# Optimization experiments

Measured on AMD Instinct MI355X. Metric: run time of the kernel, lower is better.

The kernel has to match this reference:

```python
import jax, jax.numpy as jnp
import numpy as np

B, D, T, V = 16, 128, 4096, 1024


def setup_inputs() -> dict:
    key = jax.random.key(0)
    k1, k2 = jax.random.split(key)
    latents = jax.random.normal(k1, (B, D, T), dtype=jnp.float32)
    codebook = jax.random.normal(k2, (V, D), dtype=jnp.float32)  # code_embed.weight
    return {"latents": latents, "codebook": codebook}


def reference(latents, codebook):
    # decode(): latents (B, D, T) -> (B, T, D); nearest code under L2 (torch.cdist + argmin)
    x = jnp.transpose(latents, (0, 2, 1))  # (B, T, D)
    x_sq = jnp.sum(x * x, axis=-1, keepdims=True)          # (B, T, 1)
    c_sq = jnp.sum(codebook * codebook, axis=-1)           # (V,)
    cross = jnp.einsum('btd,vd->btv', x, codebook)         # (B, T, V) -- the fusion target
    d2 = x_sq - 2.0 * cross + c_sq                         # (B, T, V)
    codes = jnp.argmin(d2, axis=-1)                        # (B, T) int
    # quantized latents: embed the chosen codes back to (B, D, T)
    quantized = jnp.transpose(codebook[codes], (0, 2, 1))  # (B, D, T)
    return codes.astype(jnp.int32), quantized
```

## Files before the change

kernel.cpp:

```cpp
#include <hip/hip_runtime.h>

#define B_ 16
#define D_ 128
#define T_ 4096
#define V_ 1024

typedef _Float16 half8 __attribute__((ext_vector_type(8)));
typedef float float4v __attribute__((ext_vector_type(4)));


__global__ __launch_bounds__(256) void split_csq_kernel(const float* __restrict__ cb,
                                                        _Float16* __restrict__ Bh,
                                                        _Float16* __restrict__ Bl,
                                                        float* __restrict__ chsq) {
    const int g = blockIdx.x * 256 + threadIdx.x;
    const int v = g >> 4;
    const int k0 = (g & 15) << 3;
    const float* src = cb + (size_t)v * D_ + k0;
    half8 h, l;
    float s = 0.f;
#pragma unroll
    for (int j = 0; j < 8; ++j) {
        float c = src[j];
        _Float16 ch = (_Float16)c;
        h[j] = ch;
        l[j] = (_Float16)((c - (float)ch) * 2048.0f);
        s = fmaf(c, c, s);
    }
    const int kt = k0 >> 5;
    const int kk = k0 & 31;
    const size_t off = ((size_t)(kt * V_ + v)) * 32 + kk;
    *(half8*)(Bh + off) = h;
    *(half8*)(Bl + off) = l;
#pragma unroll
    for (int o = 1; o < 16; o <<= 1) s += __shfl_xor(s, o, 64);
    if ((g & 15) == 0) chsq[v] = 0.5f * s;
}

__device__ __forceinline__ void dma16(const char* g, char* lds) {
    __builtin_amdgcn_global_load_lds(
        (const __attribute__((address_space(1))) unsigned int*)g,
        (__attribute__((address_space(3))) unsigned int*)lds, 16, 0, 0);
}

__device__ __forceinline__ void dma_chunk(char* ldsbuf, const char* BhB, const char* BlB,
                                          int c, int wv, int swoff) {
#pragma unroll
    for (int j = 0; j < 2; ++j) {
        const int seg = wv * 2 + j;
        const int hl = seg >> 3;
        const int kt = (seg >> 1) & 3;
        const char* src = (hl ? BlB : BhB) + kt * 65536 + c * 2048 + j * 1024 + swoff;
        dma16(src, ldsbuf + seg * 1024);
    }
}

__global__ __launch_bounds__(512, 4) void vq_mfma(const float* __restrict__ latents,
                                                  const float* __restrict__ codebook,
                                                  const float* __restrict__ chsq,
                                                  const _Float16* __restrict__ Bh,
                                                  const _Float16* __restrict__ Bl,
                                                  float* __restrict__ out_codes,
                                                  float* __restrict__ out_q) {
    __shared__ __align__(16) char smem[69632];
    __shared__ float sChsq[V_];
    __shared__ int scode[128];
    __shared__ float sBestF[2][128];
    __shared__ int sBestV[2][128];

    const int tid = threadIdx.x;
    const int tl = tid & 63;
    const int wv = tid >> 6;
    const int wt = wv & 3;
    const int wn = wv >> 2;
    const int ln = tid & 15;
    const int q = (tid >> 4) & 3;
    const int b = blockIdx.x >> 5;
    const int t00 = (blockIdx.x & 31) << 7;

    const int swoff = ((tl >> 2) << 6) + ((((tl & 3) ^ ((tl >> 3) & 3))) << 4);
    const int qs16 = ((q ^ ((ln >> 1) & 3)) << 4);

    _Float16* AhS = (_Float16*)smem;
    _Float16* AlS = AhS + 128 * 136;

#pragma unroll
    for (int i = 0; i < V_ / 512; ++i) sChsq[tid + i * 512] = chsq[tid + i * 512];

    {
        const int arow = tid & 127;
        const int adh = tid >> 7;
        const float* xp = latents + (size_t)b * D_ * T_ + t00 + arow;
#pragma unroll
        for (int i = 0; i < 4; ++i) {
            const int d0 = adh * 32 + i * 8;
            float x[8];
#pragma unroll
            for (int j = 0; j < 8; ++j) x[j] = xp[(size_t)(d0 + j) * T_];
            half8 h, l;
#pragma unroll
            for (int j = 0; j < 8; ++j) {
                _Float16 xh = (_Float16)x[j];
                h[j] = xh;
                l[j] = (_Float16)((x[j] - (float)xh) * 2048.0f);
            }
            *(half8*)(AhS + arow * 136 + d0) = h;
            *(half8*)(AlS + arow * 136 + d0) = l;
        }
    }
    __syncthreads();

    half8 ah[4][2], al[4][2];
#pragma unroll
    for (int kt = 0; kt < 4; ++kt)
#pragma unroll
        for (int mt = 0; mt < 2; ++mt) {
            const int row = wt * 32 + mt * 16 + ln;
            ah[kt][mt] = *(const half8*)(AhS + row * 136 + kt * 32 + q * 8);
            al[kt][mt] = *(const half8*)(AlS + row * 136 + kt * 32 + q * 8);
        }
    __syncthreads();

    char* Bb = smem;
    const char* BhB = (const char*)Bh;
    const char* BlB = (const char*)Bl;

    float bestF[2][4];
    int bestv[2][4];
#pragma unroll
    for (int mt = 0; mt < 2; ++mt)
#pragma unroll
        for (int r = 0; r < 4; ++r) {
            bestF[mt][r] = 3.0e38f;
            bestv[mt][r] = 0;
        }

    dma_chunk(Bb + 0 * 16384, BhB, BlB, 0, wv, swoff);
    dma_chunk(Bb + 1 * 16384, BhB, BlB, 1, wv, swoff);
    dma_chunk(Bb + 2 * 16384, BhB, BlB, 2, wv, swoff);

    for (int c = 0; c < 32; ++c) {
        asm volatile("s_waitcnt vmcnt(4)" ::: "memory");
        __builtin_amdgcn_s_barrier();
        asm volatile("" ::: "memory");

        dma_chunk(Bb + ((c + 3) & 3) * 16384, BhB, BlB, (c + 3) & 31, wv, swoff);

        const char* buf = Bb + (c & 3) * 16384;
        float4v acc1[2], acc2[2];
#pragma unroll
        for (int mt = 0; mt < 2; ++mt) {
            acc1[mt] = (float4v){0.f, 0.f, 0.f, 0.f};
            acc2[mt] = (float4v){0.f, 0.f, 0.f, 0.f};
        }
        __builtin_amdgcn_s_setprio(1);
#pragma unroll
        for (int kt = 0; kt < 4; ++kt) {
            const int o = kt * 2048 + (wn * 16 + ln) * 64 + qs16;
            const half8 bh = *(const half8*)(buf + o);
            const half8 bl = *(const half8*)(buf + 8192 + o);
#pragma unroll
            for (int mt = 0; mt < 2; ++mt) {
                acc1[mt] = __builtin_amdgcn_mfma_f32_16x16x32_f16(ah[kt][mt], bh,
                                                                  acc1[mt], 0, 0, 0);
                acc2[mt] = __builtin_amdgcn_mfma_f32_16x16x32_f16(ah[kt][mt], bl,
                                                                  acc2[mt], 0, 0, 0);
                acc2[mt] = __builtin_amdgcn_mfma_f32_16x16x32_f16(al[kt][mt], bh,
                                                                  acc2[mt], 0, 0, 0);
            }
        }
        __builtin_amdgcn_s_setprio(0);
        {
            const int n = c * 32 + wn * 16 + ln;
            const float csq = sChsq[n];
#pragma unroll
            for (int mt = 0; mt < 2; ++mt)
#pragma unroll
                for (int r = 0; r < 4; ++r) {
                    const float score =
                        csq - (acc1[mt][r] + acc2[mt][r] * (1.0f / 2048.0f));
                    if (score < bestF[mt][r]) {
                        bestF[mt][r] = score;
                        bestv[mt][r] = n;
                    }
                }
        }
    }

#pragma unroll
    for (int off = 1; off < 16; off <<= 1) {
#pragma unroll
        for (int mt = 0; mt < 2; ++mt)
#pragma unroll
            for (int r = 0; r < 4; ++r) {
                const float of = __shfl_xor(bestF[mt][r], off, 64);
                const int ov = __shfl_xor(bestv[mt][r], off, 64);
                if (of < bestF[mt][r] || (of == bestF[mt][r] && ov < bestv[mt][r])) {
                    bestF[mt][r] = of;
                    bestv[mt][r] = ov;
                }
            }
    }

    if (ln == 0) {
#pragma unroll
        for (int mt = 0; mt < 2; ++mt)
#pragma unroll
            for (int r = 0; r < 4; ++r) {
                const int m = wt * 32 + mt * 16 + q * 4 + r;
                sBestF[wn][m] = bestF[mt][r];
                sBestV[wn][m] = bestv[mt][r];
            }
    }
    __syncthreads();

    if (tid < 128) {
        const float f0 = sBestF[0][tid];
        const float f1 = sBestF[1][tid];
        const int v0 = sBestV[0][tid];
        const int v1 = sBestV[1][tid];
        const int vb = (f1 < f0 || (f1 == f0 && v1 < v0)) ? v1 : v0;
        scode[tid] = vb;
        out_codes[(size_t)b * T_ + t00 + tid] = (float)vb;
    }
    __syncthreads();

    {
        const int row = tid & 127;
        const int dq = tid >> 7;
        const int code = scode[row];
        const float* crow = codebook + (size_t)code * D_;
        float* qp = out_q + (size_t)b * D_ * T_ + t00 + row;
#pragma unroll
        for (int i = 0; i < 32; ++i) {
            const int d = dq * 32 + i;
            qp[(size_t)d * T_] = crow[d];
        }
    }
}

extern "C" void kernel_launch(void* const* d_in, const int* in_sizes, int n_in,
                              void* d_out, int out_size, void* d_ws, size_t ws_size,
                              hipStream_t stream) {
    const float* latents = (const float*)d_in[0];
    const float* codebook = (const float*)d_in[1];

    float* out_codes = (float*)d_out;
    float* out_q = (float*)d_out + B_ * T_;

    float* chsq = (float*)d_ws;
    _Float16* Bh = (_Float16*)((char*)d_ws + 4096);
    _Float16* Bl = (_Float16*)((char*)d_ws + 4096 + 262144);

    split_csq_kernel<<<(V_ * 16) / 256, 256, 0, stream>>>(codebook, Bh, Bl, chsq);
    vq_mfma<<<(B_ * T_) / 128, 512, 0, stream>>>(latents, codebook, chsq, Bh, Bl,
                                                 out_codes, out_q);
}
```

Measured before the change: 137.1 us.

## Process two codebook chunks per barrier and fold -|c|^2 into accumulator init

The main loop now handles two 32-code chunks per iteration. It waits on vmcnt(0) with one barrier per pair instead of one per chunk, and prefetch depth drops from three chunks to two. The -|c|^2 term now seeds the MFMA accumulator, so the argmin becomes an argmax over the accumulated value and a subtract per element goes away. The occupancy hint in launch_bounds is removed, which lets the compiler use more registers but may reduce waves per CU, and the full vmcnt wait can expose more load latency.

```diff
diff --git a/kernel.cpp b/kernel.cpp
--- a/kernel.cpp
+++ b/kernel.cpp
@@ -55,17 +55,17 @@
     }
 }
 
-__global__ __launch_bounds__(512, 4) void vq_mfma(const float* __restrict__ latents,
-                                                  const float* __restrict__ codebook,
-                                                  const float* __restrict__ chsq,
-                                                  const _Float16* __restrict__ Bh,
-                                                  const _Float16* __restrict__ Bl,
-                                                  float* __restrict__ out_codes,
-                                                  float* __restrict__ out_q) {
+__global__ __launch_bounds__(512) void vq_mfma(const float* __restrict__ latents,
+                                               const float* __restrict__ codebook,
+                                               const float* __restrict__ chsq,
+                                               const _Float16* __restrict__ Bh,
+                                               const _Float16* __restrict__ Bl,
+                                               float* __restrict__ out_codes,
+                                               float* __restrict__ out_q) {
     __shared__ __align__(16) char smem[69632];
     __shared__ float sChsq[V_];
     __shared__ int scode[128];
-    __shared__ float sBestF[2][128];
+    __shared__ float sBestM[2][128];
     __shared__ int sBestV[2][128];
 
     const int tid = threadIdx.x;
@@ -125,63 +125,91 @@
     const char* BhB = (const char*)Bh;
     const char* BlB = (const char*)Bl;
 
-    float bestF[2][4];
+    float bestM[2][4];
     int bestv[2][4];
 #pragma unroll
     for (int mt = 0; mt < 2; ++mt)
 #pragma unroll
         for (int r = 0; r < 4; ++r) {
-            bestF[mt][r] = 3.0e38f;
+            bestM[mt][r] = -3.0e38f;
             bestv[mt][r] = 0;
         }
 
     dma_chunk(Bb + 0 * 16384, BhB, BlB, 0, wv, swoff);
     dma_chunk(Bb + 1 * 16384, BhB, BlB, 1, wv, swoff);
-    dma_chunk(Bb + 2 * 16384, BhB, BlB, 2, wv, swoff);
-
-    for (int c = 0; c < 32; ++c) {
-        asm volatile("s_waitcnt vmcnt(4)" ::: "memory");
+
+    for (int i = 0; i < 16; ++i) {
+        const int c0 = 2 * i, c1 = 2 * i + 1;
+        asm volatile("s_waitcnt vmcnt(0)" ::: "memory");
         __builtin_amdgcn_s_barrier();
         asm volatile("" ::: "memory");
 
-        dma_chunk(Bb + ((c + 3) & 3) * 16384, BhB, BlB, (c + 3) & 31, wv, swoff);
-
-        const char* buf = Bb + (c & 3) * 16384;
-        float4v acc1[2], acc2[2];
+        dma_chunk(Bb + ((c0 + 2) & 3) * 16384, BhB, BlB, (c0 + 2) & 31, wv, swoff);
+        dma_chunk(Bb + ((c1 + 2) & 3) * 16384, BhB, BlB, (c1 + 2) & 31, wv, swoff);
+
+        const char* buf0 = Bb + (c0 & 3) * 16384;
+        const char* buf1 = Bb + (c1 & 3) * 16384;
+        const float csq0 = sChsq[c0 * 32 + wn * 16 + ln];
+        const float csq1 = sChsq[c1 * 32 + wn * 16 + ln];
+
+        float4v a1A[2], a2A[2], a1B[2], a2B[2];
 #pragma unroll
         for (int mt = 0; mt < 2; ++mt) {
-            acc1[mt] = (float4v){0.f, 0.f, 0.f, 0.f};
-            acc2[mt] = (float4v){0.f, 0.f, 0.f, 0.f};
-        }
+            a1A[mt] = (float4v){-csq0, -csq0, -csq0, -csq0};
+            a2A[mt] = (float4v){0.f, 0.f, 0.f, 0.f};
+            a1B[mt] = (float4v){-csq1, -csq1, -csq1, -csq1};
+            a2B[mt] = (float4v){0.f, 0.f, 0.f, 0.f};
+        }
+
         __builtin_amdgcn_s_setprio(1);
 #pragma unroll
         for (int kt = 0; kt < 4; ++kt) {
             const int o = kt * 2048 + (wn * 16 + ln) * 64 + qs16;
-            const half8 bh = *(const half8*)(buf + o);
-            const half8 bl = *(const half8*)(buf + 8192 + o);
+            const half8 bh = *(const half8*)(buf0 + o);
+            const half8 bl = *(const half8*)(buf0 + 8192 + o);
 #pragma unroll
             for (int mt = 0; mt < 2; ++mt) {
-                acc1[mt] = __builtin_amdgcn_mfma_f32_16x16x32_f16(ah[kt][mt], bh,
-                                                                  acc1[mt], 0, 0, 0);
-                acc2[mt] = __builtin_amdgcn_mfma_f32_16x16x32_f16(ah[kt][mt], bl,
-                                                                  acc2[mt], 0, 0, 0);
-                acc2[mt] = __builtin_amdgcn_mfma_f32_16x16x32_f16(al[kt][mt], bh,
-                                                                  acc2[mt], 0, 0, 0);
+                a1A[mt] = __builtin_amdgcn_mfma_f32_16x16x32_f16(ah[kt][mt], bh,
+                                                                 a1A[mt], 0, 0, 0);
+                a2A[mt] = __builtin_amdgcn_mfma_f32_16x16x32_f16(ah[kt][mt], bl,
+                                                                 a2A[mt], 0, 0, 0);
+                a2A[mt] = __builtin_amdgcn_mfma_f32_16x16x32_f16(al[kt][mt], bh,
+                                                                 a2A[mt], 0, 0, 0);
+            }
+        }
+#pragma unroll
+        for (int kt = 0; kt < 4; ++kt) {
+            const int o = kt * 2048 + (wn * 16 + ln) * 64 + qs16;
+            const half8 bh = *(const half8*)(buf1 + o);
+            const half8 bl = *(const half8*)(buf1 + 8192 + o);
+#pragma unroll
+            for (int mt = 0; mt < 2; ++mt) {
+                a1B[mt] = __builtin_amdgcn_mfma_f32_16x16x32_f16(ah[kt][mt], bh,
+                                                                 a1B[mt], 0, 0, 0);
+                a2B[mt] = __builtin_amdgcn_mfma_f32_16x16x32_f16(ah[kt][mt], bl,
+                                                                 a2B[mt], 0, 0, 0);
+                a2B[mt] = __builtin_amdgcn_mfma_f32_16x16x32_f16(al[kt][mt], bh,
+                                                                 a2B[mt], 0, 0, 0);
             }
         }
         __builtin_amdgcn_s_setprio(0);
+
         {
-            const int n = c * 32 + wn * 16 + ln;
-            const float csq = sChsq[n];
+            const int n0 = c0 * 32 + wn * 16 + ln;
+            const int n1 = c1 * 32 + wn * 16 + ln;
 #pragma unroll
             for (int mt = 0; mt < 2; ++mt)
 #pragma unroll
                 for (int r = 0; r < 4; ++r) {
-                    const float score =
-                        csq - (acc1[mt][r] + acc2[mt][r] * (1.0f / 2048.0f));
-                    if (score < bestF[mt][r]) {
-                        bestF[mt][r] = score;
-                        bestv[mt][r] = n;
+                    const float mA = a1A[mt][r] + a2A[mt][r] * (1.0f / 2048.0f);
+                    if (mA > bestM[mt][r]) {
+                        bestM[mt][r] = mA;
+                        bestv[mt][r] = n0;
+                    }
+                    const float mB = a1B[mt][r] + a2B[mt][r] * (1.0f / 2048.0f);
+                    if (mB > bestM[mt][r]) {
+                        bestM[mt][r] = mB;
+                        bestv[mt][r] = n1;
                     }
                 }
         }
@@ -193,10 +221,10 @@
         for (int mt = 0; mt < 2; ++mt)
 #pragma unroll
             for (int r = 0; r < 4; ++r) {
-                const float of = __shfl_xor(bestF[mt][r], off, 64);
+                const float om = __shfl_xor(bestM[mt][r], off, 64);
                 const int ov = __shfl_xor(bestv[mt][r], off, 64);
-                if (of < bestF[mt][r] || (of == bestF[mt][r] && ov < bestv[mt][r])) {
-                    bestF[mt][r] = of;
+                if (om > bestM[mt][r] || (om == bestM[mt][r] && ov < bestv[mt][r])) {
+                    bestM[mt][r] = om;
                     bestv[mt][r] = ov;
                 }
             }
@@ -208,18 +236,18 @@
 #pragma unroll
             for (int r = 0; r < 4; ++r) {
                 const int m = wt * 32 + mt * 16 + q * 4 + r;
-                sBestF[wn][m] = bestF[mt][r];
+                sBestM[wn][m] = bestM[mt][r];
                 sBestV[wn][m] = bestv[mt][r];
             }
     }
     __syncthreads();
 
     if (tid < 128) {
-        const float f0 = sBestF[0][tid];
-        const float f1 = sBestF[1][tid];
+        const float m0 = sBestM[0][tid];
+        const float m1 = sBestM[1][tid];
         const int v0 = sBestV[0][tid];
         const int v1 = sBestV[1][tid];
-        const int vb = (f1 < f0 || (f1 == f0 && v1 < v0)) ? v1 : v0;
+        const int vb = (m1 > m0 || (m1 == m0 && v1 < v0)) ? v1 : v0;
         scode[tid] = vb;
         out_codes[(size_t)b * T_ + t00 + tid] = (float)vb;
     }
```

Measured after the change: 141.9 us. +3.4%, slower.

## Load codebook fragments directly from global into registers, dropping LDS staging

Applied to the files above, without the earlier changes.

Replaces the LDS-staged multi-buffered DMA of codebook hi/lo chunks, along with its per-iteration barriers, with direct per-thread global loads into a 4-deep register ring that prefetches two k-steps ahead. The aim is to remove barrier synchronization and LDS traffic, relying on L2 to serve the codebook, which is shared by every block. In exchange, each wave issues its own global loads, gives up the cross-wave sharing that LDS provided, and uses more registers. The occupancy hint in launch_bounds is also dropped.

```diff
diff --git a/kernel.cpp b/kernel.cpp
--- a/kernel.cpp
+++ b/kernel.cpp
@@ -37,31 +37,13 @@
     if ((g & 15) == 0) chsq[v] = 0.5f * s;
 }
 
-__device__ __forceinline__ void dma16(const char* g, char* lds) {
-    __builtin_amdgcn_global_load_lds(
-        (const __attribute__((address_space(1))) unsigned int*)g,
-        (__attribute__((address_space(3))) unsigned int*)lds, 16, 0, 0);
-}
-
-__device__ __forceinline__ void dma_chunk(char* ldsbuf, const char* BhB, const char* BlB,
-                                          int c, int wv, int swoff) {
-#pragma unroll
-    for (int j = 0; j < 2; ++j) {
-        const int seg = wv * 2 + j;
-        const int hl = seg >> 3;
-        const int kt = (seg >> 1) & 3;
-        const char* src = (hl ? BlB : BhB) + kt * 65536 + c * 2048 + j * 1024 + swoff;
-        dma16(src, ldsbuf + seg * 1024);
-    }
-}
-
-__global__ __launch_bounds__(512, 4) void vq_mfma(const float* __restrict__ latents,
-                                                  const float* __restrict__ codebook,
-                                                  const float* __restrict__ chsq,
-                                                  const _Float16* __restrict__ Bh,
-                                                  const _Float16* __restrict__ Bl,
-                                                  float* __restrict__ out_codes,
-                                                  float* __restrict__ out_q) {
+__global__ __launch_bounds__(512) void vq_mfma(const float* __restrict__ latents,
+                                               const float* __restrict__ codebook,
+                                               const float* __restrict__ chsq,
+                                               const _Float16* __restrict__ Bh,
+                                               const _Float16* __restrict__ Bl,
+                                               float* __restrict__ out_codes,
+                                               float* __restrict__ out_q) {
     __shared__ __align__(16) char smem[69632];
     __shared__ float sChsq[V_];
     __shared__ int scode[128];
@@ -78,9 +60,6 @@
     const int b = blockIdx.x >> 5;
     const int t00 = (blockIdx.x & 31) << 7;
 
-    const int swoff = ((tl >> 2) << 6) + ((((tl & 3) ^ ((tl >> 3) & 3))) << 4);
-    const int qs16 = ((q ^ ((ln >> 1) & 3)) << 4);
-
     _Float16* AhS = (_Float16*)smem;
     _Float16* AlS = AhS + 128 * 136;
 
@@ -119,11 +98,21 @@
             ah[kt][mt] = *(const half8*)(AhS + row * 136 + kt * 32 + q * 8);
             al[kt][mt] = *(const half8*)(AlS + row * 136 + kt * 32 + q * 8);
         }
-    __syncthreads();
-
-    char* Bb = smem;
+
     const char* BhB = (const char*)Bh;
     const char* BlB = (const char*)Bl;
+    const int rowoff = (wn * 16 + ln) * 64 + q * 16;
+
+    half8 pbh[4], pbl[4];
+    {
+        const int o0 = rowoff;
+        const int o1 = 65536 + rowoff;
+        pbh[0] = *(const half8*)(BhB + o0);
+        pbl[0] = *(const half8*)(BlB + o0);
+        pbh[1] = *(const half8*)(BhB + o1);
+        pbl[1] = *(const half8*)(BlB + o1);
+    }
+    __syncthreads();
 
     float bestF[2][4];
     int bestv[2][4];
@@ -135,41 +124,33 @@
             bestv[mt][r] = 0;
         }
 
-    dma_chunk(Bb + 0 * 16384, BhB, BlB, 0, wv, swoff);
-    dma_chunk(Bb + 1 * 16384, BhB, BlB, 1, wv, swoff);
-    dma_chunk(Bb + 2 * 16384, BhB, BlB, 2, wv, swoff);
-
     for (int c = 0; c < 32; ++c) {
-        asm volatile("s_waitcnt vmcnt(4)" ::: "memory");
-        __builtin_amdgcn_s_barrier();
-        asm volatile("" ::: "memory");
-
-        dma_chunk(Bb + ((c + 3) & 3) * 16384, BhB, BlB, (c + 3) & 31, wv, swoff);
-
-        const char* buf = Bb + (c & 3) * 16384;
         float4v acc1[2], acc2[2];
 #pragma unroll
         for (int mt = 0; mt < 2; ++mt) {
             acc1[mt] = (float4v){0.f, 0.f, 0.f, 0.f};
             acc2[mt] = (float4v){0.f, 0.f, 0.f, 0.f};
         }
-        __builtin_amdgcn_s_setprio(1);
 #pragma unroll
         for (int kt = 0; kt < 4; ++kt) {
-            const int o = kt * 2048 + (wn * 16 + ln) * 64 + qs16;
-            const half8 bh = *(const half8*)(buf + o);
-            const half8 bl = *(const half8*)(buf + 8192 + o);
+            {
+                const int s2 = (c * 4 + kt + 2) & 127;
+                const int o = ((s2 & 3) << 16) + ((s2 >> 2) << 11) + rowoff;
+                pbh[(kt + 2) & 3] = *(const half8*)(BhB + o);
+                pbl[(kt + 2) & 3] = *(const half8*)(BlB + o);
+            }
+            __builtin_amdgcn_s_setprio(1);
 #pragma unroll
             for (int mt = 0; mt < 2; ++mt) {
-                acc1[mt] = __builtin_amdgcn_mfma_f32_16x16x32_f16(ah[kt][mt], bh,
-                                                                  acc1[mt], 0, 0, 0);
-                acc2[mt] = __builtin_amdgcn_mfma_f32_16x16x32_f16(ah[kt][mt], bl,
-                                                                  acc2[mt], 0, 0, 0);
-                acc2[mt] = __builtin_amdgcn_mfma_f32_16x16x32_f16(al[kt][mt], bh,
-                                                                  acc2[mt], 0, 0, 0);
-            }
-        }
-        __builtin_amdgcn_s_setprio(0);
+                acc1[mt] = __builtin_amdgcn_mfma_f32_16x16x32_f16(
+                    ah[kt][mt], pbh[kt], acc1[mt], 0, 0, 0);
+                acc2[mt] = __builtin_amdgcn_mfma_f32_16x16x32_f16(
+                    ah[kt][mt], pbl[kt], acc2[mt], 0, 0, 0);
+                acc2[mt] = __builtin_amdgcn_mfma_f32_16x16x32_f16(
+                    al[kt][mt], pbh[kt], acc2[mt], 0, 0, 0);
+            }
+            __builtin_amdgcn_s_setprio(0);
+        }
         {
             const int n = c * 32 + wn * 16 + ln;
             const float csq = sChsq[n];
```

New measurement: 155.1 us. 1.13x slower.
